# Kernel optimization log

Measured on AMD Instinct MI355X. Metric: run time of the kernel, lower is better.

Reference implementation:

```python
import jax, jax.numpy as jnp
import numpy as np

H = 4096
V = 32000
BT = 2048
IGNORE_INDEX = -100
WEIGHT_HARD = 0.5
WEIGHT_SOFT = 0.5
EPS = 1e-12  # F.normalize eps


def setup_inputs() -> dict:
    key = jax.random.key(0)
    k0, k1, k2, k3, k4 = jax.random.split(key, 5)
    student = jax.random.normal(k0, (BT, H // 2), dtype=jnp.float32)
    teacher = jax.random.normal(k1, (BT, H), dtype=jnp.float32)
    W_student = jax.random.normal(k2, (V, H // 2), dtype=jnp.float32) * (1.0 / np.sqrt(H // 2))
    W_teacher = jax.random.normal(k3, (V, H), dtype=jnp.float32) * (1.0 / np.sqrt(H))
    target = jax.random.randint(k4, (BT,), 0, V, dtype=jnp.int64)
    return {"student": student, "W_student": W_student, "teacher": teacher,
            "W_teacher": W_teacher, "target": target}


def reference(student, W_student, teacher, W_teacher, target):
    # Fused linear projections to vocab space
    s_logits = jnp.einsum("bh,vh->bv", student, W_student)   # [BT, V]
    t_logits = jnp.einsum("bh,vh->bv", teacher, W_teacher)   # [BT, V]

    n = target.shape[0]
    valid = target != IGNORE_INDEX                            # [BT]

    # Hard loss: cross-entropy(student_logits, target), sum over valid / BT
    logp = jax.nn.log_softmax(s_logits, axis=-1)
    safe_tgt = jnp.where(valid, target, 0)
    nll = -jnp.take_along_axis(logp, safe_tgt[:, None], axis=-1)[:, 0]
    hard_loss = jnp.sum(jnp.where(valid, nll, 0.0)) / n

    # Soft loss: 1 - cosine_similarity(student_logits, teacher_logits) per row
    s_norm = jnp.maximum(jnp.linalg.norm(s_logits, axis=-1, keepdims=True), EPS)
    t_norm = jnp.maximum(jnp.linalg.norm(t_logits, axis=-1, keepdims=True), EPS)
    cos = jnp.sum((s_logits / s_norm) * (t_logits / t_norm), axis=-1)  # [BT]
    soft_loss = jnp.sum(1.0 - cos) / n

    return WEIGHT_HARD * hard_loss + WEIGHT_SOFT * soft_loss
```

## Files before the change

### kernel.cpp

```cpp
#include <hip/hip_runtime.h>
#include <hip/hip_bf16.h>

#define H2 2048
#define HT 4096
#define NV 32000
#define NBT 2048
#define BM 128
#define BN 128
#define BK 32
#define LDT 40
#define NVB (NV / BN)

typedef __attribute__((ext_vector_type(8))) short short8;
typedef __attribute__((ext_vector_type(8))) unsigned short ushort8;
typedef __attribute__((ext_vector_type(4))) float floatx4;

static __device__ __forceinline__ unsigned int pk_bf16(float a, float b) {
  __hip_bfloat162 h = __float22bfloat162_rn(make_float2(a, b));
  union { __hip_bfloat162 h; unsigned int u; } c;
  c.h = h;
  return c.u;
}

__global__ void cvt_bf16_kernel(const float* __restrict__ src,
                                unsigned int* __restrict__ dst, int n) {
  int i = blockIdx.x * blockDim.x + threadIdx.x;
  int base = i * 8;
  if (base >= n) return;
  float4 f0 = *(const float4*)(src + base);
  float4 f1 = *(const float4*)(src + base + 4);
  uint4 o;
  o.x = pk_bf16(f0.x, f0.y);
  o.y = pk_bf16(f0.z, f0.w);
  o.z = pk_bf16(f1.x, f1.y);
  o.w = pk_bf16(f1.z, f1.w);
  *(uint4*)(dst + i * 4) = o;
}

__global__ __launch_bounds__(256, 2) void fused_gemm_kernel(
    const unsigned short* __restrict__ sbf,
    const unsigned short* __restrict__ tbf,
    const float* __restrict__ Ws,
    const float* __restrict__ Wt,
    const int* __restrict__ target,
    float* __restrict__ part,
    float* __restrict__ s_tgt_out)
{
  __shared__ unsigned short sA[BM * LDT];
  __shared__ unsigned short sB[BN * LDT];
  __shared__ float sRed[BM][4];
  __shared__ int sTgt[BM];

  const int tid = threadIdx.x;
  const int row0 = blockIdx.x * BM;
  const int col0 = blockIdx.y * BN;
  const int lane = tid & 63;
  const int wv = tid >> 6;
  const int wr = wv >> 1;
  const int wc = wv & 1;

  if (tid < BM) {
    sTgt[tid] = target[row0 + tid];
    sRed[tid][0] = 0.f; sRed[tid][1] = 0.f;
    sRed[tid][2] = 0.f; sRed[tid][3] = 0.f;
  }

  floatx4 acc_s[4][4];
  floatx4 acc_t[4][4];
#pragma unroll
  for (int i = 0; i < 4; ++i)
#pragma unroll
    for (int j = 0; j < 4; ++j) {
      acc_s[i][j] = (floatx4){0.f, 0.f, 0.f, 0.f};
      acc_t[i][j] = (floatx4){0.f, 0.f, 0.f, 0.f};
    }

  const int sr = tid >> 1;
  const int sk = (tid & 1) << 4;

  const int mrow = lane & 15;
  const int koff = (lane >> 4) << 3;
  const int abase = (wr * 64 + mrow) * LDT + koff;
  const int bbase = (wc * 64 + mrow) * LDT + koff;

  {
    const unsigned short* ap = sbf + (size_t)(row0 + sr) * H2 + sk;
    const float* bp = Ws + (size_t)(col0 + sr) * H2 + sk;
#pragma unroll 1
    for (int k0 = 0; k0 < H2; k0 += BK) {
      ushort8 a0 = *(const ushort8*)(ap);
      ushort8 a1 = *(const ushort8*)(ap + 8);
      float4 b0 = *(const float4*)(bp);
      float4 b1 = *(const float4*)(bp + 4);
      float4 b2 = *(const float4*)(bp + 8);
      float4 b3 = *(const float4*)(bp + 12);
      ap += BK; bp += BK;
      __syncthreads();
      *(ushort8*)(&sA[sr * LDT + sk]) = a0;
      *(ushort8*)(&sA[sr * LDT + sk + 8]) = a1;
      uint4 u0, u1;
      u0.x = pk_bf16(b0.x, b0.y); u0.y = pk_bf16(b0.z, b0.w);
      u0.z = pk_bf16(b1.x, b1.y); u0.w = pk_bf16(b1.z, b1.w);
      u1.x = pk_bf16(b2.x, b2.y); u1.y = pk_bf16(b2.z, b2.w);
      u1.z = pk_bf16(b3.x, b3.y); u1.w = pk_bf16(b3.z, b3.w);
      *(uint4*)(&sB[sr * LDT + sk]) = u0;
      *(uint4*)(&sB[sr * LDT + sk + 8]) = u1;
      __syncthreads();
      short8 af[4], bfrag[4];
#pragma unroll
      for (int i = 0; i < 4; ++i)
        af[i] = *(const short8*)(&sA[abase + i * 16 * LDT]);
#pragma unroll
      for (int j = 0; j < 4; ++j)
        bfrag[j] = *(const short8*)(&sB[bbase + j * 16 * LDT]);
#pragma unroll
      for (int i = 0; i < 4; ++i)
#pragma unroll
        for (int j = 0; j < 4; ++j)
          acc_s[i][j] = __builtin_amdgcn_mfma_f32_16x16x32_bf16(
              af[i], bfrag[j], acc_s[i][j], 0, 0, 0);
    }
  }

  {
    const unsigned short* ap = tbf + (size_t)(row0 + sr) * HT + sk;
    const float* bp = Wt + (size_t)(col0 + sr) * HT + sk;
#pragma unroll 1
    for (int k0 = 0; k0 < HT; k0 += BK) {
      ushort8 a0 = *(const ushort8*)(ap);
      ushort8 a1 = *(const ushort8*)(ap + 8);
      float4 b0 = *(const float4*)(bp);
      float4 b1 = *(const float4*)(bp + 4);
      float4 b2 = *(const float4*)(bp + 8);
      float4 b3 = *(const float4*)(bp + 12);
      ap += BK; bp += BK;
      __syncthreads();
      *(ushort8*)(&sA[sr * LDT + sk]) = a0;
      *(ushort8*)(&sA[sr * LDT + sk + 8]) = a1;
      uint4 u0, u1;
      u0.x = pk_bf16(b0.x, b0.y); u0.y = pk_bf16(b0.z, b0.w);
      u0.z = pk_bf16(b1.x, b1.y); u0.w = pk_bf16(b1.z, b1.w);
      u1.x = pk_bf16(b2.x, b2.y); u1.y = pk_bf16(b2.z, b2.w);
      u1.z = pk_bf16(b3.x, b3.y); u1.w = pk_bf16(b3.z, b3.w);
      *(uint4*)(&sB[sr * LDT + sk]) = u0;
      *(uint4*)(&sB[sr * LDT + sk + 8]) = u1;
      __syncthreads();
      short8 af[4], bfrag[4];
#pragma unroll
      for (int i = 0; i < 4; ++i)
        af[i] = *(const short8*)(&sA[abase + i * 16 * LDT]);
#pragma unroll
      for (int j = 0; j < 4; ++j)
        bfrag[j] = *(const short8*)(&sB[bbase + j * 16 * LDT]);
#pragma unroll
      for (int i = 0; i < 4; ++i)
#pragma unroll
        for (int j = 0; j < 4; ++j)
          acc_t[i][j] = __builtin_amdgcn_mfma_f32_16x16x32_bf16(
              af[i], bfrag[j], acc_t[i][j], 0, 0, 0);
    }
  }

#pragma unroll
  for (int i = 0; i < 4; ++i) {
#pragma unroll
    for (int r = 0; r < 4; ++r) {
      const int row_l = wr * 64 + i * 16 + (lane >> 4) * 4 + r;
      float e = 0.f, dp = 0.f, ss = 0.f, tt = 0.f;
#pragma unroll
      for (int j = 0; j < 4; ++j) {
        float s = acc_s[i][j][r];
        float t = acc_t[i][j][r];
        e += __expf(s);
        dp += s * t;
        ss += s * s;
        tt += t * t;
        const int col_l = wc * 64 + j * 16 + (lane & 15);
        if (sTgt[row_l] == col0 + col_l) s_tgt_out[row0 + row_l] = s;
      }
#pragma unroll
      for (int off = 1; off < 16; off <<= 1) {
        e  += __shfl_xor(e,  off, 16);
        dp += __shfl_xor(dp, off, 16);
        ss += __shfl_xor(ss, off, 16);
        tt += __shfl_xor(tt, off, 16);
      }
      if ((lane & 15) == 0) {
        atomicAdd(&sRed[row_l][0], e);
        atomicAdd(&sRed[row_l][1], dp);
        atomicAdd(&sRed[row_l][2], ss);
        atomicAdd(&sRed[row_l][3], tt);
      }
    }
  }
  __syncthreads();
  if (tid < BM) {
    float* p = part + (size_t)blockIdx.y * 4 * NBT + row0 + tid;
    p[0]       = sRed[tid][0];
    p[NBT]     = sRed[tid][1];
    p[2 * NBT] = sRed[tid][2];
    p[3 * NBT] = sRed[tid][3];
  }
}

__global__ void row_loss_kernel(const float* __restrict__ part,
                                const float* __restrict__ s_tgt,
                                const int* __restrict__ target,
                                float* __restrict__ row_loss) {
  const int row = blockIdx.x * blockDim.x + threadIdx.x;
  if (row >= NBT) return;
  float e = 0.f, dp = 0.f, ss = 0.f, tt = 0.f;
  for (int v = 0; v < NVB; ++v) {
    const float* p = part + (size_t)v * 4 * NBT + row;
    e  += p[0];
    dp += p[NBT];
    ss += p[2 * NBT];
    tt += p[3 * NBT];
  }
  const float lse = logf(e);
  const int tg = target[row];
  const float st = s_tgt[row];
  const float nll = (tg != -100) ? (lse - st) : 0.f;
  const float ns = fmaxf(sqrtf(ss), 1e-12f);
  const float nt = fmaxf(sqrtf(tt), 1e-12f);
  const float c = dp / (ns * nt);
  row_loss[row] = (0.5f * nll + 0.5f * (1.f - c)) * (1.f / (float)NBT);
}

__global__ void final_reduce_kernel(const float* __restrict__ row_loss,
                                    float* __restrict__ out) {
  __shared__ float sm[4];
  float v = 0.f;
  for (int i = threadIdx.x; i < NBT; i += 256) v += row_loss[i];
#pragma unroll
  for (int off = 32; off >= 1; off >>= 1) v += __shfl_down(v, off, 64);
  if ((threadIdx.x & 63) == 0) sm[threadIdx.x >> 6] = v;
  __syncthreads();
  if (threadIdx.x == 0) out[0] = sm[0] + sm[1] + sm[2] + sm[3];
}

extern "C" void kernel_launch(void* const* d_in, const int* in_sizes, int n_in,
                              void* d_out, int out_size, void* d_ws, size_t ws_size,
                              hipStream_t stream) {
  const float* student = (const float*)d_in[0];
  const float* Ws      = (const float*)d_in[1];
  const float* teacher = (const float*)d_in[2];
  const float* Wt      = (const float*)d_in[3];
  const int*   target  = (const int*)d_in[4];

  unsigned short* sbf = (unsigned short*)d_ws;
  unsigned short* tbf = sbf + (size_t)NBT * H2;
  float* part     = (float*)(tbf + (size_t)NBT * HT);
  float* s_tgt    = part + (size_t)NVB * 4 * NBT;
  float* row_loss = s_tgt + NBT;

  {
    int n = NBT * H2;
    cvt_bf16_kernel<<<(n / 8 + 255) / 256, 256, 0, stream>>>(
        student, (unsigned int*)sbf, n);
  }
  {
    int n = NBT * HT;
    cvt_bf16_kernel<<<(n / 8 + 255) / 256, 256, 0, stream>>>(
        teacher, (unsigned int*)tbf, n);
  }

  dim3 grid(NBT / BM, NV / BN);
  fused_gemm_kernel<<<grid, 256, 0, stream>>>(sbf, tbf, Ws, Wt, target,
                                              part, s_tgt);

  row_loss_kernel<<<NBT / 256, 256, 0, stream>>>(part, s_tgt, target, row_loss);
  final_reduce_kernel<<<1, 256, 0, stream>>>(row_loss, (float*)d_out);
}
```

Baseline: 2.228 ms.

## Pre-convert weights to bf16 and stream tiles via global_load_lds

Adds a path that converts both weight matrices to bf16 in workspace up front, then runs a new GEMM kernel that loads A and B tiles directly from global memory into LDS using global_load_lds. This removes the repeated fp32 weight loads and in-loop bf16 packing that every row block previously performed, and it removes the register staging. In exchange it needs a much larger workspace, adds extra conversion passes over the weights, and drops the padded LDS stride, which may cause bank conflicts. If the workspace is too small, the old kernel is used.

```diff
diff --git a/kernel.cpp b/kernel.cpp
--- a/kernel.cpp
+++ b/kernel.cpp
@@ -20,6 +20,12 @@
   union { __hip_bfloat162 h; unsigned int u; } c;
   c.h = h;
   return c.u;
+}
+
+static __device__ __forceinline__ void gload_lds16(const void* g, void* l) {
+  __builtin_amdgcn_global_load_lds(
+      (const __attribute__((address_space(1))) unsigned int*)g,
+      (__attribute__((address_space(3))) unsigned int*)l, 16, 0, 0);
 }
 
 __global__ void cvt_bf16_kernel(const float* __restrict__ src,
@@ -37,6 +43,140 @@
   *(uint4*)(dst + i * 4) = o;
 }
 
+
+template <int K>
+static __device__ __forceinline__ void gemm_phase(
+    const unsigned short* __restrict__ act,
+    const unsigned short* __restrict__ w,
+    int row0, int col0, int tid,
+    unsigned short* sA, unsigned short* sB,
+    int abase, int bbase, floatx4 (&acc)[4][4])
+{
+  const int r0 = tid >> 2;
+  const int c0 = (tid & 3) * 8;
+  const unsigned short* a0 = act + (size_t)(row0 + r0) * K + c0;
+  const unsigned short* a1 = act + (size_t)(row0 + r0 + 64) * K + c0;
+  const unsigned short* b0 = w + (size_t)(col0 + r0) * K + c0;
+  const unsigned short* b1 = w + (size_t)(col0 + r0 + 64) * K + c0;
+  unsigned short* lA0 = sA + tid * 8;
+  unsigned short* lA1 = sA + (256 + tid) * 8;
+  unsigned short* lB0 = sB + tid * 8;
+  unsigned short* lB1 = sB + (256 + tid) * 8;
+
+#pragma unroll 1
+  for (int k0 = 0; k0 < K; k0 += BK) {
+    __syncthreads();
+    gload_lds16(a0, lA0);
+    gload_lds16(a1, lA1);
+    gload_lds16(b0, lB0);
+    gload_lds16(b1, lB1);
+    a0 += BK; a1 += BK; b0 += BK; b1 += BK;
+    __syncthreads();
+    short8 af[4], bf[4];
+#pragma unroll
+    for (int i = 0; i < 4; ++i)
+      af[i] = *(const short8*)(sA + abase + i * 16 * BK);
+#pragma unroll
+    for (int j = 0; j < 4; ++j)
+      bf[j] = *(const short8*)(sB + bbase + j * 16 * BK);
+#pragma unroll
+    for (int i = 0; i < 4; ++i)
+#pragma unroll
+      for (int j = 0; j < 4; ++j)
+        acc[i][j] = __builtin_amdgcn_mfma_f32_16x16x32_bf16(
+            af[i], bf[j], acc[i][j], 0, 0, 0);
+  }
+}
+
+__global__ __launch_bounds__(256, 2) void fused_gemm_lds_kernel(
+    const unsigned short* __restrict__ sbf,
+    const unsigned short* __restrict__ tbf,
+    const unsigned short* __restrict__ Wsb,
+    const unsigned short* __restrict__ Wtb,
+    const int* __restrict__ target,
+    float* __restrict__ part,
+    float* __restrict__ s_tgt_out)
+{
+  __shared__ unsigned short sA[BM * BK];
+  __shared__ unsigned short sB[BN * BK];
+  __shared__ float sRed[BM][4];
+  __shared__ int sTgt[BM];
+
+  const int tid = threadIdx.x;
+  const int row0 = blockIdx.x * BM;
+  const int col0 = blockIdx.y * BN;
+  const int lane = tid & 63;
+  const int wv = tid >> 6;
+  const int wr = wv >> 1;
+  const int wc = wv & 1;
+
+  if (tid < BM) {
+    sTgt[tid] = target[row0 + tid];
+    sRed[tid][0] = 0.f; sRed[tid][1] = 0.f;
+    sRed[tid][2] = 0.f; sRed[tid][3] = 0.f;
+  }
+
+  floatx4 acc_s[4][4];
+  floatx4 acc_t[4][4];
+#pragma unroll
+  for (int i = 0; i < 4; ++i)
+#pragma unroll
+    for (int j = 0; j < 4; ++j) {
+      acc_s[i][j] = (floatx4){0.f, 0.f, 0.f, 0.f};
+      acc_t[i][j] = (floatx4){0.f, 0.f, 0.f, 0.f};
+    }
+
+  const int mrow = lane & 15;
+  const int koff = (lane >> 4) * 8;
+  const int abase = (wr * 64 + mrow) * BK + koff;
+  const int bbase = (wc * 64 + mrow) * BK + koff;
+
+  gemm_phase<H2>(sbf, Wsb, row0, col0, tid, sA, sB, abase, bbase, acc_s);
+  gemm_phase<HT>(tbf, Wtb, row0, col0, tid, sA, sB, abase, bbase, acc_t);
+
+#pragma unroll
+  for (int i = 0; i < 4; ++i) {
+#pragma unroll
+    for (int r = 0; r < 4; ++r) {
+      const int row_l = wr * 64 + i * 16 + (lane >> 4) * 4 + r;
+      float e = 0.f, dp = 0.f, ss = 0.f, tt = 0.f;
+#pragma unroll
+      for (int j = 0; j < 4; ++j) {
+        float s = acc_s[i][j][r];
+        float t = acc_t[i][j][r];
+        e += __expf(s);
+        dp += s * t;
+        ss += s * s;
+        tt += t * t;
+        const int col_l = wc * 64 + j * 16 + (lane & 15);
+        if (sTgt[row_l] == col0 + col_l) s_tgt_out[row0 + row_l] = s;
+      }
+#pragma unroll
+      for (int off = 1; off < 16; off <<= 1) {
+        e  += __shfl_xor(e,  off, 16);
+        dp += __shfl_xor(dp, off, 16);
+        ss += __shfl_xor(ss, off, 16);
+        tt += __shfl_xor(tt, off, 16);
+      }
+      if ((lane & 15) == 0) {
+        atomicAdd(&sRed[row_l][0], e);
+        atomicAdd(&sRed[row_l][1], dp);
+        atomicAdd(&sRed[row_l][2], ss);
+        atomicAdd(&sRed[row_l][3], tt);
+      }
+    }
+  }
+  __syncthreads();
+  if (tid < BM) {
+    float* p = part + (size_t)blockIdx.y * 4 * NBT + row0 + tid;
+    p[0]       = sRed[tid][0];
+    p[NBT]     = sRed[tid][1];
+    p[2 * NBT] = sRed[tid][2];
+    p[3 * NBT] = sRed[tid][3];
+  }
+}
+
+
 __global__ __launch_bounds__(256, 2) void fused_gemm_kernel(
     const unsigned short* __restrict__ sbf,
     const unsigned short* __restrict__ tbf,
@@ -77,7 +217,6 @@
 
   const int sr = tid >> 1;
   const int sk = (tid & 1) << 4;
-
   const int mrow = lane & 15;
   const int koff = (lane >> 4) << 3;
   const int abase = (wr * 64 + mrow) * LDT + koff;
@@ -121,7 +260,6 @@
               af[i], bfrag[j], acc_s[i][j], 0, 0, 0);
     }
   }
-
   {
     const unsigned short* ap = tbf + (size_t)(row0 + sr) * HT + sk;
     const float* bp = Wt + (size_t)(col0 + sr) * HT + sk;
@@ -203,6 +341,7 @@
   }
 }
 
+
 __global__ void row_loss_kernel(const float* __restrict__ part,
                                 const float* __restrict__ s_tgt,
                                 const int* __restrict__ target,
@@ -248,27 +387,56 @@
   const float* Wt      = (const float*)d_in[3];
   const int*   target  = (const int*)d_in[4];
 
-  unsigned short* sbf = (unsigned short*)d_ws;
-  unsigned short* tbf = sbf + (size_t)NBT * H2;
-  float* part     = (float*)(tbf + (size_t)NBT * HT);
-  float* s_tgt    = part + (size_t)NVB * 4 * NBT;
-  float* row_loss = s_tgt + NBT;
-
-  {
-    int n = NBT * H2;
-    cvt_bf16_kernel<<<(n / 8 + 255) / 256, 256, 0, stream>>>(
-        student, (unsigned int*)sbf, n);
-  }
-  {
-    int n = NBT * HT;
-    cvt_bf16_kernel<<<(n / 8 + 255) / 256, 256, 0, stream>>>(
-        teacher, (unsigned int*)tbf, n);
-  }
-
-  dim3 grid(NBT / BM, NV / BN);
-  fused_gemm_kernel<<<grid, 256, 0, stream>>>(sbf, tbf, Ws, Wt, target,
-                                              part, s_tgt);
-
-  row_loss_kernel<<<NBT / 256, 256, 0, stream>>>(part, s_tgt, target, row_loss);
-  final_reduce_kernel<<<1, 256, 0, stream>>>(row_loss, (float*)d_out);
-}
+  const size_t nS  = (size_t)NBT * H2;
+  const size_t nT  = (size_t)NBT * HT;
+  const size_t nWs = (size_t)NV * H2;
+  const size_t nWt = (size_t)NV * HT;
+  const size_t nPart = (size_t)NVB * 4 * NBT;
+
+  const size_t ws_needed_big =
+      (nS + nT + nWs + nWt) * 2 + (nPart + 2 * NBT) * 4;
+
+  if (ws_size >= ws_needed_big) {
+    unsigned short* sbf = (unsigned short*)d_ws;
+    unsigned short* tbf = sbf + nS;
+    unsigned short* Wsb = tbf + nT;
+    unsigned short* Wtb = Wsb + nWs;
+    float* part     = (float*)(Wtb + nWt);
+    float* s_tgt    = part + nPart;
+    float* row_loss = s_tgt + NBT;
+
+    cvt_bf16_kernel<<<(int)(nS / 8 / 256), 256, 0, stream>>>(
+        student, (unsigned int*)sbf, (int)nS);
+    cvt_bf16_kernel<<<(int)(nT / 8 / 256), 256, 0, stream>>>(
+        teacher, (unsigned int*)tbf, (int)nT);
+    cvt_bf16_kernel<<<(int)(nWs / 8 / 256), 256, 0, stream>>>(
+        Ws, (unsigned int*)Wsb, (int)nWs);
+    cvt_bf16_kernel<<<(int)(nWt / 8 / 256), 256, 0, stream>>>(
+        Wt, (unsigned int*)Wtb, (int)nWt);
+
+    dim3 grid(NBT / BM, NV / BN);
+    fused_gemm_lds_kernel<<<grid, 256, 0, stream>>>(
+        sbf, tbf, Wsb, Wtb, target, part, s_tgt);
+
+    row_loss_kernel<<<NBT / 256, 256, 0, stream>>>(part, s_tgt, target, row_loss);
+    final_reduce_kernel<<<1, 256, 0, stream>>>(row_loss, (float*)d_out);
+  } else {
+    unsigned short* sbf = (unsigned short*)d_ws;
+    unsigned short* tbf = sbf + nS;
+    float* part     = (float*)(tbf + nT);
+    float* s_tgt    = part + nPart;
+    float* row_loss = s_tgt + NBT;
+
+    cvt_bf16_kernel<<<(int)(nS / 8 / 256), 256, 0, stream>>>(
+        student, (unsigned int*)sbf, (int)nS);
+    cvt_bf16_kernel<<<(int)(nT / 8 / 256), 256, 0, stream>>>(
+        teacher, (unsigned int*)tbf, (int)nT);
+
+    dim3 grid(NBT / BM, NV / BN);
+    fused_gemm_kernel<<<grid, 256, 0, stream>>>(sbf, tbf, Ws, Wt, target,
+                                                part, s_tgt);
+
+    row_loss_kernel<<<NBT / 256, 256, 0, stream>>>(part, s_tgt, target, row_loss);
+    final_reduce_kernel<<<1, 256, 0, stream>>>(row_loss, (float*)d_out);
+  }
+}
```

New measurement: 1.999 ms. -10.3%, faster.
